# Optimization experiments

Hardware: AMD Instinct MI355X
Metric: run time of the kernel (lower is better)

The kernel has to match this reference:

```python
import jax, jax.numpy as jnp
import numpy as np

N, E = 50000, 800000
NFEAT, NHID, NCLASS = 128, 64, 40
NLAYERS = 4
DT, ALPHA, GAMMA = 1.0, 1.0, 1.0


def setup_inputs() -> dict:
    key = jax.random.key(0)
    ks = jax.random.split(key, 12)
    s = 1.0 / np.sqrt(NHID)
    inp = {
        'x': jax.random.normal(ks[0], (N, NFEAT), jnp.float32),
        'edge_index': jax.random.randint(ks[1], (2, E), 0, N, jnp.int64),
        # params stored as [in, out] matrices (torch Linear weight transposed)
        'enc_W': jax.random.uniform(ks[2], (NFEAT, NHID), jnp.float32, -s, s),
        'enc_b': jnp.zeros((NHID,), jnp.float32),
        'conv_W': jax.random.uniform(ks[3], (NHID, NHID), jnp.float32, -s, s),
        'conv_b': jnp.zeros((NHID,), jnp.float32),
        'res_W': jax.random.uniform(ks[4], (NHID, NHID), jnp.float32, -s, s),
        'res_b': jnp.zeros((NHID,), jnp.float32),
        'weight_mlp': jax.random.uniform(ks[5], (NHID, NHID), jnp.float32, -s, s),
        'lamda1': jnp.float32(1.0),
        'dec_W': jax.random.uniform(ks[6], (NHID, NCLASS), jnp.float32, -s, s),
        'dec_b': jnp.zeros((NCLASS,), jnp.float32),
    }
    return inp


def reference(x, edge_index, enc_W, enc_b, conv_W, conv_b, res_W, res_b,
              weight_mlp, lamda1, dec_W, dec_b):
    src, dst = edge_index[0], edge_index[1]
    # GCN symmetric normalization with self-loops (PyG GCNConv default)
    deg = jax.ops.segment_sum(jnp.ones((E,), x.dtype), dst, num_segments=N) + 1.0
    dinv = jax.lax.rsqrt(deg)                      # [N]
    enorm = (dinv[src] * dinv[dst])[:, None]       # [E,1]
    self_norm = (dinv * dinv)[:, None]             # [N,1]

    Y = jax.nn.relu(x @ enc_W + enc_b)             # [N,H]
    X = Y
    for _ in range(NLAYERS):
        Xs, Xd = X[src], X[dst]                    # [E,H] gathers
        x_new = jax.nn.relu((Xs - Xd) @ weight_mlp) * Xd
        ax3 = jax.ops.segment_sum(x_new, dst, num_segments=N)  # [N,H]
        # GCNConv: normalized aggregation of X@W plus self-loop, then bias
        xw = X @ conv_W
        conv = (jax.ops.segment_sum(xw[src] * enorm, dst, num_segments=N)
                + xw * self_norm + conv_b)
        # residual v1: -res(conv.lin(X)) = -(X@W_conv @ W_res + b_res)
        res = -(xw @ res_W + res_b)
        Y = Y + DT * (jax.nn.relu(conv + res) - ALPHA * Y - GAMMA * X)
        X = X + DT * (Y + lamda1 * ax3)
    return X @ dec_W + dec_b
```

## Files before the change

kernel.cpp:

```cpp
#include <hip/hip_runtime.h>

constexpr int H   = 64;
constexpr int NF  = 128;
constexpr int NC  = 40;
constexpr int CAP = 96;

typedef __attribute__((ext_vector_type(8))) short short8;
typedef __attribute__((ext_vector_type(4))) float f32x4;

constexpr int FRAG_ENC = 1536;
constexpr int FRAG_DEC = 3584;
constexpr int FRAG_TOT = 4352;

__device__ __forceinline__ unsigned int f2bf(float f) {
  unsigned int u = __float_as_uint(f);
  return (u + 0x7fffu + ((u >> 16) & 1u)) >> 16;
}
__device__ __forceinline__ float bf_lo(unsigned int v) { return __uint_as_float(v << 16); }
__device__ __forceinline__ float bf_hi(unsigned int v) { return __uint_as_float(v & 0xffff0000u); }
__device__ __forceinline__ short8 ld_frag(const uint4* frag, int idx) {
  uint4 u = frag[idx];
  short8 r; __builtin_memcpy(&r, &u, 16); return r;
}

__global__ void k_prep(const float* __restrict__ Wmlp, const float* __restrict__ Wconv,
                       const float* __restrict__ resW, const float* __restrict__ encW,
                       const float* __restrict__ decW, uint4* __restrict__ frag) {
  __shared__ float Wcr[64 * 64];
  int t = threadIdx.x;
  for (int idx = t; idx < 4096; idx += 256) {
    int k = idx >> 6, n = idx & 63;
    float s = 0.0f;
    for (int j = 0; j < 64; ++j) s = fmaf(Wconv[k * 64 + j], resW[j * 64 + n], s);
    Wcr[idx] = s;
  }
  __syncthreads();
  for (int it = t; it < 1536; it += 256) {
    int lane = it & 63;
    int kb = (it >> 6) & 1;
    int nb = (it >> 7) & 3;
    int w  = (it >> 9);
    int col = nb * 16 + (lane & 15);
    int k0 = kb * 32 + (lane >> 4) * 8;
    unsigned int h[8];
    for (int i = 0; i < 8; ++i) {
      float v;
      if (w == 2)      v = Wcr[(k0 + i) * 64 + col];
      else if (w == 1) v = Wconv[(k0 + i) * 64 + col];
      else             v = Wmlp[(k0 + i) * 64 + col];
      h[i] = f2bf(v);
    }
    uint4 u; u.x = h[0] | (h[1] << 16); u.y = h[2] | (h[3] << 16);
    u.z = h[4] | (h[5] << 16); u.w = h[6] | (h[7] << 16);
    frag[it] = u;
  }
  for (int it = t; it < 2048; it += 256) {
    int lane = it & 63;
    int kb = (it >> 6) & 3;
    int nb = (it >> 8) & 3;
    int hh = (it >> 10);
    int col = nb * 16 + (lane & 15);
    int k0 = kb * 32 + (lane >> 4) * 8;
    unsigned int h[8];
    for (int i = 0; i < 8; ++i) {
      float v = encW[(k0 + i) * H + col];
      unsigned int hb = f2bf(v);
      if (hh == 0) h[i] = hb;
      else         h[i] = f2bf(v - __uint_as_float(hb << 16));
    }
    uint4 u; u.x = h[0] | (h[1] << 16); u.y = h[2] | (h[3] << 16);
    u.z = h[4] | (h[5] << 16); u.w = h[6] | (h[7] << 16);
    frag[FRAG_ENC + it] = u;
  }
  for (int it = t; it < 768; it += 256) {
    int lane = it & 63;
    int kb = (it >> 6) & 1;
    int hn = it >> 7;
    int nb = hn % 3, hh = hn / 3;
    int col = nb * 16 + (lane & 15);
    int k0 = kb * 32 + (lane >> 4) * 8;
    unsigned int h[8];
    for (int i = 0; i < 8; ++i) {
      float v = (col < NC) ? decW[(k0 + i) * NC + col] : 0.0f;
      unsigned int hb = f2bf(v);
      if (hh == 0) h[i] = hb;
      else         h[i] = f2bf(v - __uint_as_float(hb << 16));
    }
    uint4 u; u.x = h[0] | (h[1] << 16); u.y = h[2] | (h[3] << 16);
    u.z = h[4] | (h[5] << 16); u.w = h[6] | (h[7] << 16);
    frag[FRAG_DEC + it] = u;
  }
}

__global__ void __launch_bounds__(256)
k_buildenc(const float* __restrict__ x, const uint4* __restrict__ frag,
           const float* __restrict__ encb, float* __restrict__ X,
           const int* __restrict__ src, const int* __restrict__ dst,
           int* __restrict__ counts, unsigned short* __restrict__ srcs,
           int N, int E) {
  int nchunks = (E + 1023) >> 10;
  if ((int)blockIdx.x < nchunks) {
    int base = (blockIdx.x << 10) + threadIdx.x;
    int d[4], s[4], slot[4];
#pragma unroll
    for (int j = 0; j < 4; ++j) {
      int e = base + j * 256;
      bool v = e < E;
      d[j] = v ? dst[e] : -1;
      s[j] = v ? src[e] : 0;
    }
#pragma unroll
    for (int j = 0; j < 4; ++j)
      slot[j] = (d[j] >= 0) ? atomicAdd(&counts[d[j]], 1) : CAP;
#pragma unroll
    for (int j = 0; j < 4; ++j)
      if (d[j] >= 0 && slot[j] < CAP) srcs[d[j] * CAP + slot[j]] = (unsigned short)s[j];
  }
  int lane = threadIdx.x & 63;
  int row = lane & 15, g = lane >> 4;
  int wv = (blockIdx.x * blockDim.x + threadIdx.x) >> 6;
  int nwv = (gridDim.x * blockDim.x) >> 6;
  float bias[4];
#pragma unroll
  for (int nb = 0; nb < 4; ++nb) bias[nb] = encb[nb * 16 + row];
  int nrb = (N + 15) >> 4;
  for (int rb = wv; rb < nrb; rb += nwv) {
    int n0 = rb << 4;
    int rload = n0 + row; if (rload > N - 1) rload = N - 1;
    const float* xp = x + (size_t)rload * NF + g * 8;
    f32x4 acc[4];
#pragma unroll
    for (int nb = 0; nb < 4; ++nb) acc[nb] = (f32x4){bias[nb], bias[nb], bias[nb], bias[nb]};
#pragma unroll
    for (int kb = 0; kb < 4; ++kb) {
      float4 a0 = *(const float4*)(xp + kb * 32);
      float4 a1 = *(const float4*)(xp + kb * 32 + 4);
      float xv[8] = {a0.x, a0.y, a0.z, a0.w, a1.x, a1.y, a1.z, a1.w};
      short8 Ahi, Alo;
#pragma unroll
      for (int i = 0; i < 8; ++i) {
        unsigned int hb = f2bf(xv[i]);
        Ahi[i] = (short)hb;
        Alo[i] = (short)f2bf(xv[i] - __uint_as_float(hb << 16));
      }
#pragma unroll
      for (int nb = 0; nb < 4; ++nb) {
        short8 Bh = ld_frag(frag, FRAG_ENC + ((0 * 4 + nb) * 4 + kb) * 64 + lane);
        short8 Bl = ld_frag(frag, FRAG_ENC + ((1 * 4 + nb) * 4 + kb) * 64 + lane);
        acc[nb] = __builtin_amdgcn_mfma_f32_16x16x32_bf16(Ahi, Bh, acc[nb], 0, 0, 0);
        acc[nb] = __builtin_amdgcn_mfma_f32_16x16x32_bf16(Alo, Bh, acc[nb], 0, 0, 0);
        acc[nb] = __builtin_amdgcn_mfma_f32_16x16x32_bf16(Ahi, Bl, acc[nb], 0, 0, 0);
      }
    }
#pragma unroll
    for (int nb = 0; nb < 4; ++nb) {
      int col = nb * 16 + row;
#pragma unroll
      for (int j = 0; j < 4; ++j) {
        int n = n0 + g * 4 + j;
        if (n < N) X[(size_t)n * H + col] = fmaxf(acc[nb][j], 0.0f);
      }
    }
  }
}

__global__ void __launch_bounds__(256, 2)
k_xform(const float* __restrict__ X, const uint4* __restrict__ frag,
        const float* __restrict__ resb, const int* __restrict__ counts,
        unsigned int* __restrict__ xmwq, unsigned short* __restrict__ rbuf, int N) {
  int lane = threadIdx.x & 63;
  int row = lane & 15, g = lane >> 4;
  int wv = (blockIdx.x * blockDim.x + threadIdx.x) >> 6;
  int nwv = (gridDim.x * blockDim.x) >> 6;

  short8 B[3][4][2];
#pragma unroll
  for (int w = 0; w < 3; ++w)
#pragma unroll
    for (int nb = 0; nb < 4; ++nb)
#pragma unroll
      for (int kb = 0; kb < 2; ++kb)
        B[w][nb][kb] = ld_frag(frag, ((w * 4 + nb) * 2 + kb) * 64 + lane);
  float rbias[4];
#pragma unroll
  for (int nb = 0; nb < 4; ++nb) rbias[nb] = resb[nb * 16 + row];

  int nrb = (N + 15) >> 4;
  for (int rb = wv; rb < nrb; rb += nwv) {
    int n0 = rb << 4;
    int rload = n0 + row; if (rload > N - 1) rload = N - 1;
    const float* xp = X + (size_t)rload * H + g * 8;
    float xv[2][8];
    {
      float4 a0 = *(const float4*)(xp);
      float4 a1 = *(const float4*)(xp + 4);
      float4 b0 = *(const float4*)(xp + 32);
      float4 b1 = *(const float4*)(xp + 36);
      xv[0][0]=a0.x; xv[0][1]=a0.y; xv[0][2]=a0.z; xv[0][3]=a0.w;
      xv[0][4]=a1.x; xv[0][5]=a1.y; xv[0][6]=a1.z; xv[0][7]=a1.w;
      xv[1][0]=b0.x; xv[1][1]=b0.y; xv[1][2]=b0.z; xv[1][3]=b0.w;
      xv[1][4]=b1.x; xv[1][5]=b1.y; xv[1][6]=b1.z; xv[1][7]=b1.w;
    }
    short8 Ahi[2], Alo[2];
#pragma unroll
    for (int kb = 0; kb < 2; ++kb)
#pragma unroll
      for (int i = 0; i < 8; ++i) {
        float v = xv[kb][i];
        unsigned int hb = f2bf(v);
        Ahi[kb][i] = (short)hb;
        Alo[kb][i] = (short)f2bf(v - __uint_as_float(hb << 16));
      }
    f32x4 am[4], ac[4], ar[4];
#pragma unroll
    for (int nb = 0; nb < 4; ++nb) {
      am[nb] = (f32x4){0.f, 0.f, 0.f, 0.f};
      ac[nb] = (f32x4){0.f, 0.f, 0.f, 0.f};
      ar[nb] = (f32x4){rbias[nb], rbias[nb], rbias[nb], rbias[nb]};
    }
#pragma unroll
    for (int nb = 0; nb < 4; ++nb)
#pragma unroll
      for (int kb = 0; kb < 2; ++kb) {
        am[nb] = __builtin_amdgcn_mfma_f32_16x16x32_bf16(Ahi[kb], B[0][nb][kb], am[nb], 0, 0, 0);
        am[nb] = __builtin_amdgcn_mfma_f32_16x16x32_bf16(Alo[kb], B[0][nb][kb], am[nb], 0, 0, 0);
        ac[nb] = __builtin_amdgcn_mfma_f32_16x16x32_bf16(Ahi[kb], B[1][nb][kb], ac[nb], 0, 0, 0);
        ac[nb] = __builtin_amdgcn_mfma_f32_16x16x32_bf16(Alo[kb], B[1][nb][kb], ac[nb], 0, 0, 0);
        ar[nb] = __builtin_amdgcn_mfma_f32_16x16x32_bf16(Ahi[kb], B[2][nb][kb], ar[nb], 0, 0, 0);
        ar[nb] = __builtin_amdgcn_mfma_f32_16x16x32_bf16(Alo[kb], B[2][nb][kb], ar[nb], 0, 0, 0);
      }
    float dn4[4];
#pragma unroll
    for (int j = 0; j < 4; ++j) {
      int n = n0 + g * 4 + j; if (n > N - 1) n = N - 1;
      dn4[j] = rsqrtf((float)counts[n] + 1.0f);
    }
#pragma unroll
    for (int nb = 0; nb < 4; ++nb) {
      int col = nb * 16 + row;
#pragma unroll
      for (int j = 0; j < 4; ++j) {
        int n = n0 + g * 4 + j;
        if (n < N) {
          xmwq[(size_t)n * H + col] = f2bf(am[nb][j]) | (f2bf(ac[nb][j] * dn4[j]) << 16);
          rbuf[(size_t)n * H + col] = (unsigned short)f2bf(ar[nb][j]);
        }
      }
    }
  }
}

template<int DOX>
__global__ void __launch_bounds__(256)
k_updx(const unsigned int* __restrict__ xmwq_in, const unsigned short* __restrict__ rbuf_in,
       const unsigned short* __restrict__ srcs, const int* __restrict__ counts,
       const float* __restrict__ convb, const float* __restrict__ lam1,
       float* __restrict__ X, const uint4* __restrict__ frag,
       const float* __restrict__ resb,
       unsigned int* __restrict__ xmwq_out, unsigned short* __restrict__ rbuf_out, int N) {
  __shared__ float sX[16][68];
  int lane = threadIdx.x & 63;
  int w = threadIdx.x >> 6;
  int row = lane & 15, gg = lane >> 4;
  float cb = convb[lane];
  float lam = lam1[0];
  short8 Bw[3][2];
  float rbias = 0.0f;
  if (DOX) {
#pragma unroll
    for (int m = 0; m < 3; ++m)
#pragma unroll
      for (int kb = 0; kb < 2; ++kb)
        Bw[m][kb] = ld_frag(frag, ((m * 4 + w) * 2 + kb) * 64 + lane);
    rbias = resb[w * 16 + row];
  }
  int ngrp = (N + 15) >> 4;
  for (int g = blockIdx.x; g < ngrp; g += gridDim.x) {
#pragma unroll
    for (int j = 0; j < 4; ++j) {
      int nig = w * 4 + j;
      int n = g * 16 + nig;
      bool act = n < N;
      int nn = act ? n : N - 1;
      size_t rowo = (size_t)nn * H + lane;
      unsigned int own = xmwq_in[rowo];
      float xmd = bf_lo(own), xwsd = bf_hi(own);
      float r = __uint_as_float((unsigned int)rbuf_in[rowo] << 16);
      float Xd = X[rowo];
      int cntfull = counts[nn];
      float dn = rsqrtf((float)cntfull + 1.0f);
      int cnt = cntfull < CAP ? cntfull : CAP;
      int sv0 = (lane < cnt) ? (int)srcs[nn * CAP + lane] : 0;
      int sv1 = (64 + lane < cnt) ? (int)srcs[nn * CAP + 64 + lane] : 0;
      float acc3 = 0.0f, accC = 0.0f;
      for (int e = 0; e < cnt; e += 16) {
        unsigned int v[16]; float m[16];
#pragma unroll
        for (int q = 0; q < 16; ++q) {
          int eq = e + q;
          bool valid = eq < cnt;
          int s = valid ? ((eq < 64) ? __builtin_amdgcn_readlane(sv0, eq)
                                     : __builtin_amdgcn_readlane(sv1, eq - 64))
                        : 0;
          v[q] = xmwq_in[(size_t)s * H + lane];
          m[q] = valid ? 1.0f : 0.0f;
        }
#pragma unroll
        for (int q = 0; q < 16; ++q) {
          acc3 += m[q] * fmaxf(bf_lo(v[q]) - xmd, 0.0f);
          accC += m[q] * bf_hi(v[q]);
        }
      }
      float conv = fmaf(dn, accC + xwsd, cb);
      float R = fmaxf(conv - r, 0.0f);
      float Xnew = R + lam * (acc3 * Xd);
      if (act) X[rowo] = Xnew;
      if (DOX) sX[nig][lane] = act ? Xnew : 0.0f;
    }
    if (DOX) {
      __syncthreads();
      short8 Ahi[2], Alo[2];
#pragma unroll
      for (int kb = 0; kb < 2; ++kb) {
        float4 a0 = *(const float4*)&sX[row][kb * 32 + gg * 8];
        float4 a1 = *(const float4*)&sX[row][kb * 32 + gg * 8 + 4];
        float xv[8] = {a0.x, a0.y, a0.z, a0.w, a1.x, a1.y, a1.z, a1.w};
#pragma unroll
        for (int i = 0; i < 8; ++i) {
          unsigned int hb = f2bf(xv[i]);
          Ahi[kb][i] = (short)hb;
          Alo[kb][i] = (short)f2bf(xv[i] - __uint_as_float(hb << 16));
        }
      }
      f32x4 am = (f32x4){0.f, 0.f, 0.f, 0.f};
      f32x4 ac = (f32x4){0.f, 0.f, 0.f, 0.f};
      f32x4 ar = (f32x4){rbias, rbias, rbias, rbias};
#pragma unroll
      for (int kb = 0; kb < 2; ++kb) {
        am = __builtin_amdgcn_mfma_f32_16x16x32_bf16(Ahi[kb], Bw[0][kb], am, 0, 0, 0);
        am = __builtin_amdgcn_mfma_f32_16x16x32_bf16(Alo[kb], Bw[0][kb], am, 0, 0, 0);
        ac = __builtin_amdgcn_mfma_f32_16x16x32_bf16(Ahi[kb], Bw[1][kb], ac, 0, 0, 0);
        ac = __builtin_amdgcn_mfma_f32_16x16x32_bf16(Alo[kb], Bw[1][kb], ac, 0, 0, 0);
        ar = __builtin_amdgcn_mfma_f32_16x16x32_bf16(Ahi[kb], Bw[2][kb], ar, 0, 0, 0);
        ar = __builtin_amdgcn_mfma_f32_16x16x32_bf16(Alo[kb], Bw[2][kb], ar, 0, 0, 0);
      }
      int col = w * 16 + row;
#pragma unroll
      for (int j = 0; j < 4; ++j) {
        int n = g * 16 + gg * 4 + j;
        if (n < N) {
          float dn = rsqrtf((float)counts[n] + 1.0f);
          xmwq_out[(size_t)n * H + col] = f2bf(am[j]) | (f2bf(ac[j] * dn) << 16);
          rbuf_out[(size_t)n * H + col] = (unsigned short)f2bf(ar[j]);
        }
      }
      __syncthreads();
    }
  }
}

__global__ void __launch_bounds__(256)
k_dec(const float* __restrict__ X, const uint4* __restrict__ frag,
      const float* __restrict__ decb, float* __restrict__ out, int N) {
  int lane = threadIdx.x & 63;
  int row = lane & 15, g = lane >> 4;
  int wv = (blockIdx.x * blockDim.x + threadIdx.x) >> 6;
  int nwv = (gridDim.x * blockDim.x) >> 6;
  float bias[3];
#pragma unroll
  for (int nb = 0; nb < 3; ++nb) {
    int col = nb * 16 + row;
    bias[nb] = (col < NC) ? decb[col] : 0.0f;
  }
  int nrb = (N + 15) >> 4;
  for (int rb = wv; rb < nrb; rb += nwv) {
    int n0 = rb << 4;
    int rload = n0 + row; if (rload > N - 1) rload = N - 1;
    const float* xp = X + (size_t)rload * H + g * 8;
    f32x4 acc[3];
#pragma unroll
    for (int nb = 0; nb < 3; ++nb) acc[nb] = (f32x4){bias[nb], bias[nb], bias[nb], bias[nb]};
#pragma unroll
    for (int kb = 0; kb < 2; ++kb) {
      float4 a0 = *(const float4*)(xp + kb * 32);
      float4 a1 = *(const float4*)(xp + kb * 32 + 4);
      float xv[8] = {a0.x, a0.y, a0.z, a0.w, a1.x, a1.y, a1.z, a1.w};
      short8 Ahi, Alo;
#pragma unroll
      for (int i = 0; i < 8; ++i) {
        unsigned int hb = f2bf(xv[i]);
        Ahi[i] = (short)hb;
        Alo[i] = (short)f2bf(xv[i] - __uint_as_float(hb << 16));
      }
#pragma unroll
      for (int nb = 0; nb < 3; ++nb) {
        short8 Bh = ld_frag(frag, FRAG_DEC + ((0 * 3 + nb) * 2 + kb) * 64 + lane);
        short8 Bl = ld_frag(frag, FRAG_DEC + ((1 * 3 + nb) * 2 + kb) * 64 + lane);
        acc[nb] = __builtin_amdgcn_mfma_f32_16x16x32_bf16(Ahi, Bh, acc[nb], 0, 0, 0);
        acc[nb] = __builtin_amdgcn_mfma_f32_16x16x32_bf16(Alo, Bh, acc[nb], 0, 0, 0);
        acc[nb] = __builtin_amdgcn_mfma_f32_16x16x32_bf16(Ahi, Bl, acc[nb], 0, 0, 0);
      }
    }
#pragma unroll
    for (int nb = 0; nb < 3; ++nb) {
      int col = nb * 16 + row;
      if (col < NC) {
#pragma unroll
        for (int j = 0; j < 4; ++j) {
          int n = n0 + g * 4 + j;
          if (n < N) out[(size_t)n * NC + col] = acc[nb][j];
        }
      }
    }
  }
}

extern "C" void kernel_launch(void* const* d_in, const int* in_sizes, int n_in,
                              void* d_out, int out_size, void* d_ws, size_t ws_size,
                              hipStream_t stream) {
  const float* x    = (const float*)d_in[0];
  const int*   ei   = (const int*)d_in[1];
  const float* encW = (const float*)d_in[2];
  const float* encb = (const float*)d_in[3];
  const float* convW= (const float*)d_in[4];
  const float* convb= (const float*)d_in[5];
  const float* resW = (const float*)d_in[6];
  const float* resb = (const float*)d_in[7];
  const float* wmlp = (const float*)d_in[8];
  const float* lam1 = (const float*)d_in[9];
  const float* decW = (const float*)d_in[10];
  const float* decb = (const float*)d_in[11];
  int N = in_sizes[0] / NF;
  int E = in_sizes[1] / 2;
  const int* src = ei;
  const int* dst = ei + E;

  char* ws = (char*)d_ws;
  size_t off = 0;
  auto alloc = [&](size_t bytes) -> void* {
    void* p = ws + off;
    off = (off + bytes + 255) & ~(size_t)255;
    return p;
  };
  int*            counts = (int*)alloc((size_t)N * 4);
  unsigned short* srcs   = (unsigned short*)alloc((size_t)N * CAP * 2);
  float*          X      = (float*)alloc((size_t)N * H * 4);
  unsigned int*   xmwqA  = (unsigned int*)alloc((size_t)N * H * 4);
  unsigned int*   xmwqB  = (unsigned int*)alloc((size_t)N * H * 4);
  unsigned short* rbufA  = (unsigned short*)alloc((size_t)N * H * 2);
  unsigned short* rbufB  = (unsigned short*)alloc((size_t)N * H * 2);
  uint4*          frag   = (uint4*)alloc((size_t)FRAG_TOT * 16);

  hipMemsetAsync(counts, 0, (size_t)N * 4, stream);

  const int tb = 256;
  k_prep<<<1, tb, 0, stream>>>(wmlp, convW, resW, encW, decW, frag);
  k_buildenc<<<2048, tb, 0, stream>>>(x, frag, encb, X, src, dst, counts, srcs, N, E);
  k_xform<<<784, tb, 0, stream>>>(X, frag, resb, counts, xmwqA, rbufA, N);
  k_updx<1><<<1024, tb, 0, stream>>>(xmwqA, rbufA, srcs, counts, convb, lam1, X,
                                     frag, resb, xmwqB, rbufB, N);
  k_updx<1><<<1024, tb, 0, stream>>>(xmwqB, rbufB, srcs, counts, convb, lam1, X,
                                     frag, resb, xmwqA, rbufA, N);
  k_updx<1><<<1024, tb, 0, stream>>>(xmwqA, rbufA, srcs, counts, convb, lam1, X,
                                     frag, resb, xmwqB, rbufB, N);
  k_updx<0><<<2048, tb, 0, stream>>>(xmwqB, rbufB, srcs, counts, convb, lam1, X,
                                     frag, resb, xmwqA, rbufA, N);
  k_dec<<<784, tb, 0, stream>>>(X, frag, decb, (float*)d_out, N);
}
```

Measured before the change: 300.3 us.

## Partition edge bucketing by destination range and launch one block per node group

The edge-bucketing phase now splits edges into 2048-edge chunks and gives each chunk to eight blocks. Each block handles only destinations in one eighth of the node range, so the atomics and slot writes from a block land in a narrower address region and are meant to hit cache more often. The cost is that every block rereads its chunk's dst array, eight times the index traffic in total. The update kernels now launch one block per 16-node group instead of a fixed 1024 or 2048 blocks, which assumes the kernel uses a grid-stride loop that still covers all nodes.

```diff
diff --git a/kernel.cpp b/kernel.cpp
--- a/kernel.cpp
+++ b/kernel.cpp
@@ -4,6 +4,7 @@
 constexpr int NF  = 128;
 constexpr int NC  = 40;
 constexpr int CAP = 96;
+constexpr int ECHUNK = 2048;
 
 typedef __attribute__((ext_vector_type(8))) short short8;
 typedef __attribute__((ext_vector_type(4))) float f32x4;
@@ -98,23 +99,24 @@
            const int* __restrict__ src, const int* __restrict__ dst,
            int* __restrict__ counts, unsigned short* __restrict__ srcs,
            int N, int E) {
-  int nchunks = (E + 1023) >> 10;
-  if ((int)blockIdx.x < nchunks) {
-    int base = (blockIdx.x << 10) + threadIdx.x;
-    int d[4], s[4], slot[4];
-#pragma unroll
-    for (int j = 0; j < 4; ++j) {
-      int e = base + j * 256;
-      bool v = e < E;
-      d[j] = v ? dst[e] : -1;
-      s[j] = v ? src[e] : 0;
-    }
-#pragma unroll
-    for (int j = 0; j < 4; ++j)
-      slot[j] = (d[j] >= 0) ? atomicAdd(&counts[d[j]], 1) : CAP;
-#pragma unroll
-    for (int j = 0; j < 4; ++j)
-      if (d[j] >= 0 && slot[j] < CAP) srcs[d[j] * CAP + slot[j]] = (unsigned short)s[j];
+  int nch = (E + ECHUNK - 1) / ECHUNK;
+  int nbuild = nch * 8;
+  if ((int)blockIdx.x < nbuild) {
+    int chunk = blockIdx.x >> 3;
+    int cls   = blockIdx.x & 7;
+    int CLS = (N + 7) >> 3;
+    int lo = cls * CLS;
+    int hi = lo + CLS; if (hi > N) hi = N;
+    int base = chunk * ECHUNK;
+    int lim = E - base; if (lim > ECHUNK) lim = ECHUNK;
+    for (int i = threadIdx.x; i < lim; i += 256) {
+      int e = base + i;
+      int d = dst[e];
+      if (d >= lo && d < hi) {
+        int slot = atomicAdd(&counts[d], 1);
+        if (slot < CAP) srcs[d * CAP + slot] = (unsigned short)src[e];
+      }
+    }
   }
   int lane = threadIdx.x & 63;
   int row = lane & 15, g = lane >> 4;
@@ -455,15 +457,17 @@
 
   const int tb = 256;
   k_prep<<<1, tb, 0, stream>>>(wmlp, convW, resW, encW, decW, frag);
-  k_buildenc<<<2048, tb, 0, stream>>>(x, frag, encb, X, src, dst, counts, srcs, N, E);
+  int nch = (E + ECHUNK - 1) / ECHUNK;
+  k_buildenc<<<nch * 8, tb, 0, stream>>>(x, frag, encb, X, src, dst, counts, srcs, N, E);
   k_xform<<<784, tb, 0, stream>>>(X, frag, resb, counts, xmwqA, rbufA, N);
-  k_updx<1><<<1024, tb, 0, stream>>>(xmwqA, rbufA, srcs, counts, convb, lam1, X,
+  int ngrp = (N + 15) >> 4;
+  k_updx<1><<<ngrp, tb, 0, stream>>>(xmwqA, rbufA, srcs, counts, convb, lam1, X,
                                      frag, resb, xmwqB, rbufB, N);
-  k_updx<1><<<1024, tb, 0, stream>>>(xmwqB, rbufB, srcs, counts, convb, lam1, X,
+  k_updx<1><<<ngrp, tb, 0, stream>>>(xmwqB, rbufB, srcs, counts, convb, lam1, X,
                                      frag, resb, xmwqA, rbufA, N);
-  k_updx<1><<<1024, tb, 0, stream>>>(xmwqA, rbufA, srcs, counts, convb, lam1, X,
+  k_updx<1><<<ngrp, tb, 0, stream>>>(xmwqA, rbufA, srcs, counts, convb, lam1, X,
                                      frag, resb, xmwqB, rbufB, N);
-  k_updx<0><<<2048, tb, 0, stream>>>(xmwqB, rbufB, srcs, counts, convb, lam1, X,
+  k_updx<0><<<ngrp, tb, 0, stream>>>(xmwqB, rbufB, srcs, counts, convb, lam1, X,
                                      frag, resb, xmwqA, rbufA, N);
   k_dec<<<784, tb, 0, stream>>>(X, frag, decb, (float*)d_out, N);
 }
```

Result: slower. 323.5 us (+7.7%).

## Parallelize weight prep and interleave neighbor gathers across four nodes per wave

Applied to the files above, without the earlier changes.

The single-block weight-prep kernel is split into a 16-block Wconv·Wres product kernel and a multi-block fragment-packing kernel, so the serial prep no longer runs on one workgroup. In the update kernel each wave now loads metadata for its four nodes up front and walks their neighbor lists together in steps of 8. This puts gathers from four nodes in flight at once, hiding memory latency better than processing one node at a time with 16 loads. The update launches also use one block per 16-node group instead of a grid-stride loop. In exchange the kernel uses more registers, which may lower occupancy, and waves branch on per-node edge counts.

```diff
diff --git a/kernel.cpp b/kernel.cpp
--- a/kernel.cpp
+++ b/kernel.cpp
@@ -23,26 +23,28 @@
   short8 r; __builtin_memcpy(&r, &u, 16); return r;
 }
 
+__global__ void k_wcr(const float* __restrict__ Wconv, const float* __restrict__ resW,
+                      float* __restrict__ Wcr) {
+  int idx = blockIdx.x * 256 + threadIdx.x;
+  int k = idx >> 6, n = idx & 63;
+  float s = 0.0f;
+  for (int j = 0; j < 64; ++j) s = fmaf(Wconv[k * 64 + j], resW[j * 64 + n], s);
+  Wcr[idx] = s;
+}
+
 __global__ void k_prep(const float* __restrict__ Wmlp, const float* __restrict__ Wconv,
-                       const float* __restrict__ resW, const float* __restrict__ encW,
+                       const float* __restrict__ Wcr, const float* __restrict__ encW,
                        const float* __restrict__ decW, uint4* __restrict__ frag) {
-  __shared__ float Wcr[64 * 64];
-  int t = threadIdx.x;
-  for (int idx = t; idx < 4096; idx += 256) {
-    int k = idx >> 6, n = idx & 63;
-    float s = 0.0f;
-    for (int j = 0; j < 64; ++j) s = fmaf(Wconv[k * 64 + j], resW[j * 64 + n], s);
-    Wcr[idx] = s;
-  }
-  __syncthreads();
-  for (int it = t; it < 1536; it += 256) {
+  int it = blockIdx.x * 256 + threadIdx.x;
+  if (it >= FRAG_TOT) return;
+  unsigned int h[8];
+  if (it < FRAG_ENC) {
     int lane = it & 63;
     int kb = (it >> 6) & 1;
     int nb = (it >> 7) & 3;
     int w  = (it >> 9);
     int col = nb * 16 + (lane & 15);
     int k0 = kb * 32 + (lane >> 4) * 8;
-    unsigned int h[8];
     for (int i = 0; i < 8; ++i) {
       float v;
       if (w == 2)      v = Wcr[(k0 + i) * 64 + col];
@@ -50,46 +52,36 @@
       else             v = Wmlp[(k0 + i) * 64 + col];
       h[i] = f2bf(v);
     }
-    uint4 u; u.x = h[0] | (h[1] << 16); u.y = h[2] | (h[3] << 16);
-    u.z = h[4] | (h[5] << 16); u.w = h[6] | (h[7] << 16);
-    frag[it] = u;
-  }
-  for (int it = t; it < 2048; it += 256) {
-    int lane = it & 63;
-    int kb = (it >> 6) & 3;
-    int nb = (it >> 8) & 3;
-    int hh = (it >> 10);
+  } else if (it < FRAG_DEC) {
+    int e = it - FRAG_ENC;
+    int lane = e & 63;
+    int kb = (e >> 6) & 3;
+    int nb = (e >> 8) & 3;
+    int hh = (e >> 10);
     int col = nb * 16 + (lane & 15);
     int k0 = kb * 32 + (lane >> 4) * 8;
-    unsigned int h[8];
     for (int i = 0; i < 8; ++i) {
       float v = encW[(k0 + i) * H + col];
       unsigned int hb = f2bf(v);
-      if (hh == 0) h[i] = hb;
-      else         h[i] = f2bf(v - __uint_as_float(hb << 16));
-    }
-    uint4 u; u.x = h[0] | (h[1] << 16); u.y = h[2] | (h[3] << 16);
-    u.z = h[4] | (h[5] << 16); u.w = h[6] | (h[7] << 16);
-    frag[FRAG_ENC + it] = u;
-  }
-  for (int it = t; it < 768; it += 256) {
-    int lane = it & 63;
-    int kb = (it >> 6) & 1;
-    int hn = it >> 7;
+      h[i] = (hh == 0) ? hb : f2bf(v - __uint_as_float(hb << 16));
+    }
+  } else {
+    int e = it - FRAG_DEC;
+    int lane = e & 63;
+    int kb = (e >> 6) & 1;
+    int hn = e >> 7;
     int nb = hn % 3, hh = hn / 3;
     int col = nb * 16 + (lane & 15);
     int k0 = kb * 32 + (lane >> 4) * 8;
-    unsigned int h[8];
     for (int i = 0; i < 8; ++i) {
       float v = (col < NC) ? decW[(k0 + i) * NC + col] : 0.0f;
       unsigned int hb = f2bf(v);
-      if (hh == 0) h[i] = hb;
-      else         h[i] = f2bf(v - __uint_as_float(hb << 16));
-    }
-    uint4 u; u.x = h[0] | (h[1] << 16); u.y = h[2] | (h[3] << 16);
-    u.z = h[4] | (h[5] << 16); u.w = h[6] | (h[7] << 16);
-    frag[FRAG_DEC + it] = u;
-  }
+      h[i] = (hh == 0) ? hb : f2bf(v - __uint_as_float(hb << 16));
+    }
+  }
+  uint4 u; u.x = h[0] | (h[1] << 16); u.y = h[2] | (h[3] << 16);
+  u.z = h[4] | (h[5] << 16); u.w = h[6] | (h[7] << 16);
+  frag[it] = u;
 }
 
 __global__ void __launch_bounds__(256)
@@ -276,46 +268,68 @@
   }
   int ngrp = (N + 15) >> 4;
   for (int g = blockIdx.x; g < ngrp; g += gridDim.x) {
+    int nn[4], cnt[4], sv0[4], sv1[4];
+    float xmd[4], xwsd[4], rr[4], Xd[4], dn[4];
+    int maxcnt = 0;
 #pragma unroll
     for (int j = 0; j < 4; ++j) {
-      int nig = w * 4 + j;
-      int n = g * 16 + nig;
+      int n = g * 16 + w * 4 + j;
       bool act = n < N;
-      int nn = act ? n : N - 1;
-      size_t rowo = (size_t)nn * H + lane;
+      nn[j] = act ? n : N - 1;
+      size_t rowo = (size_t)nn[j] * H + lane;
       unsigned int own = xmwq_in[rowo];
-      float xmd = bf_lo(own), xwsd = bf_hi(own);
-      float r = __uint_as_float((unsigned int)rbuf_in[rowo] << 16);
-      float Xd = X[rowo];
-      int cntfull = counts[nn];
-      float dn = rsqrtf((float)cntfull + 1.0f);
-      int cnt = cntfull < CAP ? cntfull : CAP;
-      int sv0 = (lane < cnt) ? (int)srcs[nn * CAP + lane] : 0;
-      int sv1 = (64 + lane < cnt) ? (int)srcs[nn * CAP + 64 + lane] : 0;
-      float acc3 = 0.0f, accC = 0.0f;
-      for (int e = 0; e < cnt; e += 16) {
-        unsigned int v[16]; float m[16];
-#pragma unroll
-        for (int q = 0; q < 16; ++q) {
-          int eq = e + q;
-          bool valid = eq < cnt;
-          int s = valid ? ((eq < 64) ? __builtin_amdgcn_readlane(sv0, eq)
-                                     : __builtin_amdgcn_readlane(sv1, eq - 64))
-                        : 0;
-          v[q] = xmwq_in[(size_t)s * H + lane];
-          m[q] = valid ? 1.0f : 0.0f;
-        }
-#pragma unroll
-        for (int q = 0; q < 16; ++q) {
-          acc3 += m[q] * fmaxf(bf_lo(v[q]) - xmd, 0.0f);
-          accC += m[q] * bf_hi(v[q]);
-        }
-      }
-      float conv = fmaf(dn, accC + xwsd, cb);
-      float R = fmaxf(conv - r, 0.0f);
-      float Xnew = R + lam * (acc3 * Xd);
-      if (act) X[rowo] = Xnew;
-      if (DOX) sX[nig][lane] = act ? Xnew : 0.0f;
+      xmd[j] = bf_lo(own); xwsd[j] = bf_hi(own);
+      rr[j] = __uint_as_float((unsigned int)rbuf_in[rowo] << 16);
+      Xd[j] = X[rowo];
+      int cf = counts[nn[j]];
+      dn[j] = rsqrtf((float)cf + 1.0f);
+      cnt[j] = cf < CAP ? cf : CAP;
+      sv0[j] = (lane < cnt[j]) ? (int)srcs[nn[j] * CAP + lane] : 0;
+      sv1[j] = (64 + lane < cnt[j]) ? (int)srcs[nn[j] * CAP + 64 + lane] : 0;
+      maxcnt = cnt[j] > maxcnt ? cnt[j] : maxcnt;
+    }
+    float acc3[4] = {0.f, 0.f, 0.f, 0.f}, accC[4] = {0.f, 0.f, 0.f, 0.f};
+    for (int e = 0; e < maxcnt; e += 8) {
+      unsigned int v[4][8];
+#pragma unroll
+      for (int j = 0; j < 4; ++j) {
+        if (e < cnt[j]) {
+#pragma unroll
+          for (int q = 0; q < 8; ++q) {
+            int eq = e + q;
+            bool valid = eq < cnt[j];
+            int s = valid ? ((eq < 64) ? __builtin_amdgcn_readlane(sv0[j], eq)
+                                       : __builtin_amdgcn_readlane(sv1[j], eq - 64))
+                          : 0;
+            v[j][q] = valid ? xmwq_in[(size_t)s * H + lane] : 0u;
+          }
+        } else {
+#pragma unroll
+          for (int q = 0; q < 8; ++q) v[j][q] = 0u;
+        }
+      }
+#pragma unroll
+      for (int j = 0; j < 4; ++j) {
+        if (e < cnt[j]) {
+#pragma unroll
+          for (int q = 0; q < 8; ++q) {
+            bool valid = (e + q) < cnt[j];
+            float m = valid ? 1.0f : 0.0f;
+            acc3[j] += m * fmaxf(bf_lo(v[j][q]) - xmd[j], 0.0f);
+            accC[j] += m * bf_hi(v[j][q]);
+          }
+        }
+      }
+    }
+#pragma unroll
+    for (int j = 0; j < 4; ++j) {
+      int n = g * 16 + w * 4 + j;
+      bool act = n < N;
+      float conv = fmaf(dn[j], accC[j] + xwsd[j], cb);
+      float R = fmaxf(conv - rr[j], 0.0f);
+      float Xnew = R + lam * (acc3[j] * Xd[j]);
+      if (act) X[(size_t)nn[j] * H + lane] = Xnew;
+      if (DOX) sX[w * 4 + j][lane] = act ? Xnew : 0.0f;
     }
     if (DOX) {
       __syncthreads();
@@ -349,8 +363,8 @@
       for (int j = 0; j < 4; ++j) {
         int n = g * 16 + gg * 4 + j;
         if (n < N) {
-          float dn = rsqrtf((float)counts[n] + 1.0f);
-          xmwq_out[(size_t)n * H + col] = f2bf(am[j]) | (f2bf(ac[j] * dn) << 16);
+          float dnn = rsqrtf((float)counts[n] + 1.0f);
+          xmwq_out[(size_t)n * H + col] = f2bf(am[j]) | (f2bf(ac[j] * dnn) << 16);
           rbuf_out[(size_t)n * H + col] = (unsigned short)f2bf(ar[j]);
         }
       }
@@ -450,20 +464,23 @@
   unsigned short* rbufA  = (unsigned short*)alloc((size_t)N * H * 2);
   unsigned short* rbufB  = (unsigned short*)alloc((size_t)N * H * 2);
   uint4*          frag   = (uint4*)alloc((size_t)FRAG_TOT * 16);
+  float*          Wcr    = (float*)alloc(64 * 64 * 4);
 
   hipMemsetAsync(counts, 0, (size_t)N * 4, stream);
 
   const int tb = 256;
-  k_prep<<<1, tb, 0, stream>>>(wmlp, convW, resW, encW, decW, frag);
+  k_wcr<<<16, tb, 0, stream>>>(convW, resW, Wcr);
+  k_prep<<<(FRAG_TOT + tb - 1) / tb, tb, 0, stream>>>(wmlp, convW, Wcr, encW, decW, frag);
   k_buildenc<<<2048, tb, 0, stream>>>(x, frag, encb, X, src, dst, counts, srcs, N, E);
   k_xform<<<784, tb, 0, stream>>>(X, frag, resb, counts, xmwqA, rbufA, N);
-  k_updx<1><<<1024, tb, 0, stream>>>(xmwqA, rbufA, srcs, counts, convb, lam1, X,
+  int ngrp = (N + 15) >> 4;
+  k_updx<1><<<ngrp, tb, 0, stream>>>(xmwqA, rbufA, srcs, counts, convb, lam1, X,
                                      frag, resb, xmwqB, rbufB, N);
-  k_updx<1><<<1024, tb, 0, stream>>>(xmwqB, rbufB, srcs, counts, convb, lam1, X,
+  k_updx<1><<<ngrp, tb, 0, stream>>>(xmwqB, rbufB, srcs, counts, convb, lam1, X,
                                      frag, resb, xmwqA, rbufA, N);
-  k_updx<1><<<1024, tb, 0, stream>>>(xmwqA, rbufA, srcs, counts, convb, lam1, X,
+  k_updx<1><<<ngrp, tb, 0, stream>>>(xmwqA, rbufA, srcs, counts, convb, lam1, X,
                                      frag, resb, xmwqB, rbufB, N);
-  k_updx<0><<<2048, tb, 0, stream>>>(xmwqB, rbufB, srcs, counts, convb, lam1, X,
+  k_updx<0><<<ngrp, tb, 0, stream>>>(xmwqB, rbufB, srcs, counts, convb, lam1, X,
                                      frag, resb, xmwqA, rbufA, N);
   k_dec<<<784, tb, 0, stream>>>(X, frag, decb, (float*)d_out, N);
 }
```

New measurement: 345.0 us. 1.15x slower.

## Parallelize weight prep across blocks and launch one block per node group

Applied to the files above, without the earlier changes.

The single-block prep kernel, which computed the Wconv·Wres product and packed all weight fragments serially, is split. A 16-block kernel now computes the product and a multi-block kernel packs one fragment per thread. The update kernels drop their grid-stride loop and launch one block per 16-node group, which removes the trailing __syncthreads. This shortens the serial prologue and removes per-iteration loop and barrier overhead. In exchange, each block reloads the weight fragments once per group instead of amortizing them over several groups, and one extra kernel launch is added.

```diff
diff --git a/kernel.cpp b/kernel.cpp
--- a/kernel.cpp
+++ b/kernel.cpp
@@ -23,26 +23,28 @@
   short8 r; __builtin_memcpy(&r, &u, 16); return r;
 }
 
+__global__ void k_wcr(const float* __restrict__ Wconv, const float* __restrict__ resW,
+                      float* __restrict__ Wcr) {
+  int idx = blockIdx.x * 256 + threadIdx.x;
+  int k = idx >> 6, n = idx & 63;
+  float s = 0.0f;
+  for (int j = 0; j < 64; ++j) s = fmaf(Wconv[k * 64 + j], resW[j * 64 + n], s);
+  Wcr[idx] = s;
+}
+
 __global__ void k_prep(const float* __restrict__ Wmlp, const float* __restrict__ Wconv,
-                       const float* __restrict__ resW, const float* __restrict__ encW,
+                       const float* __restrict__ Wcr, const float* __restrict__ encW,
                        const float* __restrict__ decW, uint4* __restrict__ frag) {
-  __shared__ float Wcr[64 * 64];
-  int t = threadIdx.x;
-  for (int idx = t; idx < 4096; idx += 256) {
-    int k = idx >> 6, n = idx & 63;
-    float s = 0.0f;
-    for (int j = 0; j < 64; ++j) s = fmaf(Wconv[k * 64 + j], resW[j * 64 + n], s);
-    Wcr[idx] = s;
-  }
-  __syncthreads();
-  for (int it = t; it < 1536; it += 256) {
+  int it = blockIdx.x * 256 + threadIdx.x;
+  if (it >= FRAG_TOT) return;
+  unsigned int h[8];
+  if (it < FRAG_ENC) {
     int lane = it & 63;
     int kb = (it >> 6) & 1;
     int nb = (it >> 7) & 3;
     int w  = (it >> 9);
     int col = nb * 16 + (lane & 15);
     int k0 = kb * 32 + (lane >> 4) * 8;
-    unsigned int h[8];
     for (int i = 0; i < 8; ++i) {
       float v;
       if (w == 2)      v = Wcr[(k0 + i) * 64 + col];
@@ -50,46 +52,36 @@
       else             v = Wmlp[(k0 + i) * 64 + col];
       h[i] = f2bf(v);
     }
-    uint4 u; u.x = h[0] | (h[1] << 16); u.y = h[2] | (h[3] << 16);
-    u.z = h[4] | (h[5] << 16); u.w = h[6] | (h[7] << 16);
-    frag[it] = u;
-  }
-  for (int it = t; it < 2048; it += 256) {
-    int lane = it & 63;
-    int kb = (it >> 6) & 3;
-    int nb = (it >> 8) & 3;
-    int hh = (it >> 10);
+  } else if (it < FRAG_DEC) {
+    int e = it - FRAG_ENC;
+    int lane = e & 63;
+    int kb = (e >> 6) & 3;
+    int nb = (e >> 8) & 3;
+    int hh = (e >> 10);
     int col = nb * 16 + (lane & 15);
     int k0 = kb * 32 + (lane >> 4) * 8;
-    unsigned int h[8];
     for (int i = 0; i < 8; ++i) {
       float v = encW[(k0 + i) * H + col];
       unsigned int hb = f2bf(v);
-      if (hh == 0) h[i] = hb;
-      else         h[i] = f2bf(v - __uint_as_float(hb << 16));
-    }
-    uint4 u; u.x = h[0] | (h[1] << 16); u.y = h[2] | (h[3] << 16);
-    u.z = h[4] | (h[5] << 16); u.w = h[6] | (h[7] << 16);
-    frag[FRAG_ENC + it] = u;
-  }
-  for (int it = t; it < 768; it += 256) {
-    int lane = it & 63;
-    int kb = (it >> 6) & 1;
-    int hn = it >> 7;
+      h[i] = (hh == 0) ? hb : f2bf(v - __uint_as_float(hb << 16));
+    }
+  } else {
+    int e = it - FRAG_DEC;
+    int lane = e & 63;
+    int kb = (e >> 6) & 1;
+    int hn = e >> 7;
     int nb = hn % 3, hh = hn / 3;
     int col = nb * 16 + (lane & 15);
     int k0 = kb * 32 + (lane >> 4) * 8;
-    unsigned int h[8];
     for (int i = 0; i < 8; ++i) {
       float v = (col < NC) ? decW[(k0 + i) * NC + col] : 0.0f;
       unsigned int hb = f2bf(v);
-      if (hh == 0) h[i] = hb;
-      else         h[i] = f2bf(v - __uint_as_float(hb << 16));
-    }
-    uint4 u; u.x = h[0] | (h[1] << 16); u.y = h[2] | (h[3] << 16);
-    u.z = h[4] | (h[5] << 16); u.w = h[6] | (h[7] << 16);
-    frag[FRAG_DEC + it] = u;
-  }
+      h[i] = (hh == 0) ? hb : f2bf(v - __uint_as_float(hb << 16));
+    }
+  }
+  uint4 u; u.x = h[0] | (h[1] << 16); u.y = h[2] | (h[3] << 16);
+  u.z = h[4] | (h[5] << 16); u.w = h[6] | (h[7] << 16);
+  frag[it] = u;
 }
 
 __global__ void __launch_bounds__(256)
@@ -274,8 +266,8 @@
         Bw[m][kb] = ld_frag(frag, ((m * 4 + w) * 2 + kb) * 64 + lane);
     rbias = resb[w * 16 + row];
   }
-  int ngrp = (N + 15) >> 4;
-  for (int g = blockIdx.x; g < ngrp; g += gridDim.x) {
+  int g = blockIdx.x;
+  {
 #pragma unroll
     for (int j = 0; j < 4; ++j) {
       int nig = w * 4 + j;
@@ -349,12 +341,11 @@
       for (int j = 0; j < 4; ++j) {
         int n = g * 16 + gg * 4 + j;
         if (n < N) {
-          float dn = rsqrtf((float)counts[n] + 1.0f);
-          xmwq_out[(size_t)n * H + col] = f2bf(am[j]) | (f2bf(ac[j] * dn) << 16);
+          float dnn = rsqrtf((float)counts[n] + 1.0f);
+          xmwq_out[(size_t)n * H + col] = f2bf(am[j]) | (f2bf(ac[j] * dnn) << 16);
           rbuf_out[(size_t)n * H + col] = (unsigned short)f2bf(ar[j]);
         }
       }
-      __syncthreads();
     }
   }
 }
@@ -450,20 +441,23 @@
   unsigned short* rbufA  = (unsigned short*)alloc((size_t)N * H * 2);
   unsigned short* rbufB  = (unsigned short*)alloc((size_t)N * H * 2);
   uint4*          frag   = (uint4*)alloc((size_t)FRAG_TOT * 16);
+  float*          Wcr    = (float*)alloc(64 * 64 * 4);
 
   hipMemsetAsync(counts, 0, (size_t)N * 4, stream);
 
   const int tb = 256;
-  k_prep<<<1, tb, 0, stream>>>(wmlp, convW, resW, encW, decW, frag);
+  k_wcr<<<16, tb, 0, stream>>>(convW, resW, Wcr);
+  k_prep<<<(FRAG_TOT + tb - 1) / tb, tb, 0, stream>>>(wmlp, convW, Wcr, encW, decW, frag);
   k_buildenc<<<2048, tb, 0, stream>>>(x, frag, encb, X, src, dst, counts, srcs, N, E);
   k_xform<<<784, tb, 0, stream>>>(X, frag, resb, counts, xmwqA, rbufA, N);
-  k_updx<1><<<1024, tb, 0, stream>>>(xmwqA, rbufA, srcs, counts, convb, lam1, X,
+  int ngrp = (N + 15) >> 4;
+  k_updx<1><<<ngrp, tb, 0, stream>>>(xmwqA, rbufA, srcs, counts, convb, lam1, X,
                                      frag, resb, xmwqB, rbufB, N);
-  k_updx<1><<<1024, tb, 0, stream>>>(xmwqB, rbufB, srcs, counts, convb, lam1, X,
+  k_updx<1><<<ngrp, tb, 0, stream>>>(xmwqB, rbufB, srcs, counts, convb, lam1, X,
                                      frag, resb, xmwqA, rbufA, N);
-  k_updx<1><<<1024, tb, 0, stream>>>(xmwqA, rbufA, srcs, counts, convb, lam1, X,
+  k_updx<1><<<ngrp, tb, 0, stream>>>(xmwqA, rbufA, srcs, counts, convb, lam1, X,
                                      frag, resb, xmwqB, rbufB, N);
-  k_updx<0><<<2048, tb, 0, stream>>>(xmwqB, rbufB, srcs, counts, convb, lam1, X,
+  k_updx<0><<<ngrp, tb, 0, stream>>>(xmwqB, rbufB, srcs, counts, convb, lam1, X,
                                      frag, resb, xmwqA, rbufA, N);
   k_dec<<<784, tb, 0, stream>>>(X, frag, decb, (float*)d_out, N);
 }
```

After: 269.3 us. 10.3% less time.
